# Kernel optimization log

Hardware: AMD Instinct MI355X
Metric: run time of the kernel (lower is better)

The kernel has to match this reference:

```python
import jax, jax.numpy as jnp
import numpy as np
from jax import lax

B = 128
NODES = 304
T_STEPS = 20
HID = 64
GCN_IN = 20
N = B * NODES            # 38912 graph nodes
E = N * 16               # 622592 edges
BN_EPS = 1e-5


def setup_inputs() -> dict:
    key = jax.random.key(0)
    ks = jax.random.split(key, 32)
    rn = lambda k, s, sc=0.1: jax.random.normal(k, s, jnp.float32) * sc
    return {
        "data_x": jax.random.normal(ks[0], (N, GCN_IN), jnp.float32),
        "edge_index": jax.random.randint(ks[1], (2, E), 0, N),
        "edge_weight": jax.random.uniform(ks[2], (E,), jnp.float32),
        "tc1_w1": rn(ks[3], (HID, 1, 1, 3)), "tc1_b1": rn(ks[4], (HID,)),
        "tc1_w2": rn(ks[5], (HID, 1, 1, 3)), "tc1_b2": rn(ks[6], (HID,)),
        "tc1_w3": rn(ks[7], (HID, 1, 1, 3)), "tc1_b3": rn(ks[8], (HID,)),
        "gcn_W0": rn(ks[9], (GCN_IN, HID)), "gcn_b0": rn(ks[10], (HID,)),
        "bn0_g": jax.random.uniform(ks[11], (HID,), jnp.float32, 0.5, 1.5), "bn0_b": rn(ks[12], (HID,)),
        "gcn_W1": rn(ks[13], (HID, HID)), "gcn_b1": rn(ks[14], (HID,)),
        "bn1_g": jax.random.uniform(ks[15], (HID,), jnp.float32, 0.5, 1.5), "bn1_b": rn(ks[16], (HID,)),
        "tc2_w1": rn(ks[17], (1, HID, 1, 3)), "tc2_b1": rn(ks[18], (1,)),
        "tc2_w2": rn(ks[19], (1, HID, 1, 3)), "tc2_b2": rn(ks[20], (1,)),
        "tc2_w3": rn(ks[21], (1, HID, 1, 3)), "tc2_b3": rn(ks[22], (1,)),
        "bn2d_g": jax.random.uniform(ks[23], (NODES,), jnp.float32, 0.5, 1.5), "bn2d_b": rn(ks[24], (NODES,)),
        "fc_W": rn(ks[25], (21 * NODES, 2048), 0.01), "fc_b": rn(ks[26], (2048,)),
        "fc4_W": rn(ks[27], (2048, 300), 0.01), "fc4_b": rn(ks[28], (300,)),
    }


def _bn(x, g, b):
    # eval-mode BatchNorm with fresh running stats (mean=0, var=1)
    return x * (g / jnp.sqrt(1.0 + BN_EPS)) + b


def _temporal_conv(X, w1, b1, w2, b2, w3, b3):
    # X: [B, T, nodes, C] -> permute to NCHW [B, C, nodes, T]
    Xp = jnp.transpose(X, (0, 3, 2, 1))
    conv = lambda w, b: lax.conv_general_dilated(
        Xp, w, (1, 1), [(0, 0), (1, 1)],
        dimension_numbers=("NCHW", "OIHW", "NCHW")) + b[None, :, None, None]
    P = conv(w1, b1)
    Q = jax.nn.sigmoid(conv(w2, b2))
    H = jax.nn.relu(P * Q + conv(w3, b3))
    return jnp.transpose(H, (0, 3, 2, 1))  # back to [B, T, nodes, C_out]


def reference(data_x, edge_index, edge_weight,
              tc1_w1, tc1_b1, tc1_w2, tc1_b2, tc1_w3, tc1_b3,
              gcn_W0, gcn_b0, bn0_g, bn0_b,
              gcn_W1, gcn_b1, bn1_g, bn1_b,
              tc2_w1, tc2_b1, tc2_w2, tc2_b2, tc2_w3, tc2_b3,
              bn2d_g, bn2d_b, fc_W, fc_b, fc4_W, fc4_b):
    n = data_x.shape[0]
    b = n // NODES

    # ---- GCN norm (sym, self-loops w=1) ----
    row, col = edge_index[0], edge_index[1]
    loop = jnp.arange(n)
    rowF = jnp.concatenate([row, loop])
    colF = jnp.concatenate([col, loop])
    ewF = jnp.concatenate([edge_weight, jnp.ones((n,), data_x.dtype)])
    deg = jax.ops.segment_sum(ewF, colF, num_segments=n)
    dinv = lax.rsqrt(jnp.maximum(deg, 1e-12))
    norm = dinv[rowF] * ewF * dinv[colF]

    def gconv(x, W, bias):
        h = x @ W
        return jax.ops.segment_sum(h[rowF] * norm[:, None], colF, num_segments=n) + bias

    x = jax.nn.relu(_bn(gconv(data_x, gcn_W0, gcn_b0), bn0_g, bn0_b))
    x = jax.nn.relu(_bn(gconv(x, gcn_W1, gcn_b1), bn1_g, bn1_b))  # [N, HID]

    # ---- temporal conv 1 ----
    X = data_x.reshape(b, T_STEPS, NODES, 1)
    T0 = _temporal_conv(X, tc1_w1, tc1_b1, tc1_w2, tc1_b2, tc1_w3, tc1_b3)  # [B,20,304,HID]

    # gcn_feature.permute(1,0).reshape(-1, 1, nodes, HID)
    gfeat = x.T.reshape(b, 1, NODES, HID)

    T = jnp.concatenate([jax.nn.relu(T0), gfeat], axis=1)  # [B, 21, 304, HID]
    T = jax.nn.relu(T)

    # ---- temporal conv 2 ----
    T = _temporal_conv(T, tc2_w1, tc2_b1, tc2_w2, tc2_b2, tc2_w3, tc2_b3)  # [B,21,304,1]

    # BatchNorm2d over node channel (axis=2 here), eval-mode running stats
    T = T * (bn2d_g / jnp.sqrt(1.0 + BN_EPS))[None, None, :, None] + bn2d_b[None, None, :, None]

    T = T.reshape(b, -1)  # [B, 6384]
    T = jax.nn.relu(T @ fc_W + fc_b)
    return T @ fc4_W + fc4_b  # [B, 300]
```

## Files before the change

kernel.cpp:

```cpp
#include <hip/hip_runtime.h>

#define NODES   304
#define BATCH   128
#define TSTEPS  20
#define HID     64
#define GCNIN   20
#define NN      (BATCH*NODES)
#define NE      (NN*16)
#define SEGSZ   (NN/4)
#define BCAP    64
#define FC1_IN  (21*NODES)
#define KP1     6400
#define FC1_OUT 2048
#define FC2_OUT 300
#define NP2     304
#define BN_EPS  1e-5f

typedef __attribute__((ext_vector_type(8))) short short8;
typedef __attribute__((ext_vector_type(4))) float f32x4;
typedef __attribute__((ext_vector_type(2))) float f32x2;

static __device__ __forceinline__ short f2bf(float x) {
    unsigned u = __float_as_uint(x);
    unsigned r = (u + 0x7FFF + ((u >> 16) & 1)) >> 16;
    return (short)r;
}
static __device__ __forceinline__ float bf2f(unsigned short v) {
    return __uint_as_float((unsigned)v << 16);
}

static __device__ __forceinline__ float fast_sigmoid(float q) {
    return __builtin_amdgcn_rcpf(1.f + __expf(-q));
}

static __device__ __forceinline__ f32x2 pk_fma(f32x2 a, f32x2 b, f32x2 c) {
    f32x2 d;
    asm("v_pk_fma_f32 %0, %1, %2, %3" : "=v"(d) : "v"(a), "v"(b), "v"(c));
    return d;
}

template <int C>
static __device__ __forceinline__ float dppadd(float v) {
    return v + __int_as_float(
        __builtin_amdgcn_update_dpp(0, __float_as_int(v), C, 0xF, 0xF, false));
}
static __device__ __forceinline__ float rsum16(float v) {
    v = dppadd<0x128>(v);
    v = dppadd<0x124>(v);
    v = dppadd<0x122>(v);
    v = dppadd<0x121>(v);
    return v;
}

__global__ void k_bucket(const int* __restrict__ ei, const float* __restrict__ ew,
                         int* __restrict__ cnt, int2* __restrict__ bucket) {
    int e = blockIdx.x * blockDim.x + threadIdx.x;
    if (e < NE) {
        int c = ei[NE + e];
        int slot = atomicAdd(&cnt[c], 1);
        if (slot < BCAP) {
            int2 v;
            v.x = ei[e];
            v.y = __float_as_int(ew[e]);
            bucket[((size_t)c << 6) + slot] = v;
        }
    }
}

__global__ __launch_bounds__(256) void k_mm20(const float* __restrict__ X,
                                              const float* __restrict__ W,
                                              const int* __restrict__ cnt,
                                              const int2* __restrict__ bucket,
                                              unsigned short* __restrict__ H,
                                              float* __restrict__ dinv) {
    int wv = threadIdx.x >> 6, f = threadIdx.x & 63;
    int n = blockIdx.x * 4 + wv;
    __shared__ float xs[4][GCNIN];
    __shared__ float rs[4][4];

    int2 be = bucket[((size_t)n << 6) + f];
    int deg = cnt[n];
    if (f < GCNIN) xs[wv][f] = X[(size_t)n * GCNIN + f];

    int dcap = deg < BCAP ? deg : BCAP;
    float wsum = (f < dcap) ? __int_as_float(be.y) : 0.f;
    wsum = rsum16(wsum);
    if ((f & 15) == 0) rs[wv][f >> 4] = wsum;
    __syncthreads();

    float dv = rsqrtf(fmaxf(1.f + rs[wv][0] + rs[wv][1] + rs[wv][2] + rs[wv][3],
                            1e-12f));
    if (f == 0) dinv[n] = dv;

    float acc = 0.f;
#pragma unroll
    for (int k = 0; k < GCNIN; k++) acc = fmaf(xs[wv][k], W[k * HID + f], acc);
    H[(size_t)n * HID + f] = (unsigned short)f2bf(acc * dv);
}

static __device__ __forceinline__ void stage_partition(
    int deg, int2 e, int f, int wv, int (*sIdx)[BCAP], float (*sWt)[BCAP],
    int& dcap) {
    dcap = deg < BCAP ? deg : BCAP;
    bool valid = f < dcap;
    int row = e.x;
    float w = __int_as_float(e.y);
    int q = (row >= SEGSZ) + (row >= 2 * SEGSZ) + (row >= 3 * SEGSZ);
    unsigned long long b0 = __ballot(valid && q == 0);
    unsigned long long b1 = __ballot(valid && q == 1);
    unsigned long long b2 = __ballot(valid && q == 2);
    unsigned long long b3 = __ballot(valid && q == 3);
    unsigned long long lmask = (1ULL << f) - 1;
    int pos = 0;
    if (q > 0) pos += __popcll(b0);
    if (q > 1) pos += __popcll(b1);
    if (q > 2) pos += __popcll(b2);
    unsigned long long mybal = (q == 0) ? b0 : (q == 1) ? b1 : (q == 2) ? b2 : b3;
    pos += __popcll(mybal & lmask);
    if (valid) {
        sIdx[wv][pos] = row;
        sWt[wv][pos] = w;
    }
}

__global__ __launch_bounds__(256) void k_gatherA(const int* __restrict__ cnt,
                                                 const int2* __restrict__ bucket,
                                                 const float* __restrict__ dinv,
                                                 const unsigned short* __restrict__ H0,
                                                 const float* __restrict__ gb,
                                                 const float* __restrict__ bng,
                                                 const float* __restrict__ bnb,
                                                 const float* __restrict__ W1,
                                                 unsigned short* __restrict__ H1) {
    int wv = threadIdx.x >> 6, f = threadIdx.x & 63;
    int c = blockIdx.x * 4 + wv;
    __shared__ int sIdx[4][BCAP];
    __shared__ float sWt[4][BCAP];
    __shared__ float xs[4][HID];

    int2 be = bucket[((size_t)c << 6) + f];
    int deg = cnt[c];
    float dc = dinv[c];
    float self = bf2f(H0[(size_t)c * HID + f]);

    int dcap;
    stage_partition(deg, be, f, wv, sIdx, sWt, dcap);
    __syncthreads();

    float acc = self;
    for (int base = 0; base < dcap; base += 16) {
        int idx[16];
        float w[16];
#pragma unroll
        for (int i = 0; i < 16; i++) {
            int l = (base + i < dcap) ? base + i : dcap - 1;
            idx[i] = sIdx[wv][l];
            w[i] = (base + i < dcap) ? sWt[wv][l] : 0.f;
        }
        float v[16];
#pragma unroll
        for (int i = 0; i < 16; i++) v[i] = bf2f(H0[(size_t)idx[i] * HID + f]);
#pragma unroll
        for (int i = 0; i < 16; i++) acc = fmaf(v[i], w[i], acc);
    }
    float scale = bng[f] * rsqrtf(1.f + BN_EPS);
    float y = fmaxf(fmaf(acc * dc + gb[f], scale, bnb[f]), 0.f);

    xs[wv][f] = y;
    __syncthreads();
    float h = 0.f;
#pragma unroll
    for (int k4 = 0; k4 < HID / 4; k4++) {
        float4 xv = *(const float4*)&xs[wv][k4 * 4];
        h = fmaf(xv.x, W1[(k4 * 4 + 0) * HID + f], h);
        h = fmaf(xv.y, W1[(k4 * 4 + 1) * HID + f], h);
        h = fmaf(xv.z, W1[(k4 * 4 + 2) * HID + f], h);
        h = fmaf(xv.w, W1[(k4 * 4 + 3) * HID + f], h);
    }
    H1[(size_t)c * HID + f] = (unsigned short)f2bf(h * dc);
}

__global__ __launch_bounds__(256) void k_gatherB(const int* __restrict__ cnt,
                                                 const int2* __restrict__ bucket,
                                                 const float* __restrict__ dinv,
                                                 const unsigned short* __restrict__ H,
                                                 const float* __restrict__ gb,
                                                 const float* __restrict__ bng,
                                                 const float* __restrict__ bnb,
                                                 float* __restrict__ XO) {
    int wv = threadIdx.x >> 6, f = threadIdx.x & 63;
    int c = blockIdx.x * 4 + wv;
    __shared__ int sIdx[4][BCAP];
    __shared__ float sWt[4][BCAP];

    int2 be = bucket[((size_t)c << 6) + f];
    int deg = cnt[c];
    float dc = dinv[c];
    float self = bf2f(H[(size_t)c * HID + f]);

    int dcap;
    stage_partition(deg, be, f, wv, sIdx, sWt, dcap);
    __syncthreads();

    float acc = self;
    for (int base = 0; base < dcap; base += 16) {
        int idx[16];
        float w[16];
#pragma unroll
        for (int i = 0; i < 16; i++) {
            int l = (base + i < dcap) ? base + i : dcap - 1;
            idx[i] = sIdx[wv][l];
            w[i] = (base + i < dcap) ? sWt[wv][l] : 0.f;
        }
        float v[16];
#pragma unroll
        for (int i = 0; i < 16; i++) v[i] = bf2f(H[(size_t)idx[i] * HID + f]);
#pragma unroll
        for (int i = 0; i < 16; i++) acc = fmaf(v[i], w[i], acc);
    }
    float scale = bng[f] * rsqrtf(1.f + BN_EPS);
    XO[(size_t)c * HID + f] = fmaxf(fmaf(acc * dc + gb[f], scale, bnb[f]), 0.f);
}

__global__ __launch_bounds__(256) void k_xpose(const float* __restrict__ x2,
                                               float* __restrict__ x2t) {
    __shared__ float tile[64][65];
    int n0 = blockIdx.x * 64;
    for (int i = threadIdx.x; i < 4096; i += 256) {
        int r = i >> 6, h = i & 63;
        tile[r][h] = x2[(size_t)(n0 + r) * 64 + h];
    }
    __syncthreads();
    for (int i = threadIdx.x; i < 4096; i += 256) {
        int h = i >> 6, c = i & 63;
        x2t[(size_t)h * NN + n0 + c] = tile[c][h];
    }
}

static __device__ __forceinline__ void load12(const float* base, f32x2 P[2][3]) {
    float4 f0 = *(const float4*)(base);
    float4 f1 = *(const float4*)(base + 4);
    float4 f2 = *(const float4*)(base + 8);
    P[0][0][0] = f0.x; P[0][0][1] = f0.w;
    P[0][1][0] = f0.y; P[0][1][1] = f1.x;
    P[0][2][0] = f0.z; P[0][2][1] = f1.y;
    P[1][0][0] = f1.z; P[1][0][1] = f2.y;
    P[1][1][0] = f1.w; P[1][1][1] = f2.z;
    P[1][2][0] = f2.x; P[1][2][1] = f2.w;
}

__global__ __launch_bounds__(256) void k_temporal2(
    const float* __restrict__ data_x, const float* __restrict__ x2t,
    const float* __restrict__ w1, const float* __restrict__ b1,
    const float* __restrict__ w2, const float* __restrict__ b2,
    const float* __restrict__ w3, const float* __restrict__ b3,
    const float* __restrict__ v1, const float* __restrict__ vb1,
    const float* __restrict__ v2, const float* __restrict__ vb2,
    const float* __restrict__ v3, const float* __restrict__ vb3,
    const float* __restrict__ bn2g, const float* __restrict__ bn2b,
    short* __restrict__ Ab) {
    int bn0 = blockIdx.x * 16;
    int b = bn0 / NODES, node0 = bn0 % NODES;
    int tid = threadIdx.x;
    int p = tid >> 4;
    int c0 = (tid & 15) << 2;
    int node = node0 + p;

    __shared__ float xs[16][22];
    __shared__ float wlds[1344];

    if (tid < 192) {
        wlds[tid] = w1[tid];
        wlds[192 + tid] = w2[tid];
        wlds[384 + tid] = w3[tid];
        wlds[576 + tid] = v1[tid];
        wlds[768 + tid] = v2[tid];
        wlds[960 + tid] = v3[tid];
    }
    if (tid < 64) {
        wlds[1152 + tid] = b1[tid];
        wlds[1216 + tid] = b2[tid];
        wlds[1280 + tid] = b3[tid];
    }
    for (int i = tid; i < 320; i += 256) {
        int t = i >> 4, pp = i & 15;
        xs[pp][t + 1] = data_x[b * (TSTEPS * NODES) + t * NODES + node0 + pp];
    }
    if (tid < 16) { xs[tid][0] = 0.f; xs[tid][21] = 0.f; }

    float cb1 = vb1[0], cb2 = vb2[0], cb3 = vb3[0];
    float s2 = bn2g[node] * rsqrtf(1.f + BN_EPS);
    float bb2 = bn2b[node];
    short* dst = Ab + (size_t)b * KP1;

    __syncthreads();

    f32x2 A1p[2][3], A2p[2][3], A3p[2][3], B1p[2], B2p[2], B3p[2];
    f32x2 U1p[2][3], U2p[2][3], U3p[2][3];
    load12(&wlds[0 + c0 * 3], A1p);
    load12(&wlds[192 + c0 * 3], A2p);
    load12(&wlds[384 + c0 * 3], A3p);
    load12(&wlds[576 + c0 * 3], U1p);
    load12(&wlds[768 + c0 * 3], U2p);
    load12(&wlds[960 + c0 * 3], U3p);
    {
        float4 t1 = *(const float4*)&wlds[1152 + c0];
        float4 t2 = *(const float4*)&wlds[1216 + c0];
        float4 t3 = *(const float4*)&wlds[1280 + c0];
        B1p[0][0] = t1.x; B1p[0][1] = t1.y; B1p[1][0] = t1.z; B1p[1][1] = t1.w;
        B2p[0][0] = t2.x; B2p[0][1] = t2.y; B2p[1][0] = t2.z; B2p[1][1] = t2.w;
        B3p[0][0] = t3.x; B3p[0][1] = t3.y; B3p[1][0] = t3.z; B3p[1][1] = t3.w;
    }

    f32x2 hA2[2] = {}, hB2[2] = {}, hC2[2];
    float xr0 = xs[p][0], xr1 = xs[p][1];

#pragma unroll
    for (int j = 0; j <= 21; j++) {
        if (j < 20) {
            float xr2 = xs[p][j + 2];
            f32x2 x0d, x1d, x2d;
            x0d[0] = xr0; x0d[1] = xr0;
            x1d[0] = xr1; x1d[1] = xr1;
            x2d[0] = xr2; x2d[1] = xr2;
#pragma unroll
            for (int cp = 0; cp < 2; cp++) {
                f32x2 pv = pk_fma(A1p[cp][2], x2d,
                            pk_fma(A1p[cp][1], x1d, pk_fma(A1p[cp][0], x0d, B1p[cp])));
                f32x2 qv = pk_fma(A2p[cp][2], x2d,
                            pk_fma(A2p[cp][1], x1d, pk_fma(A2p[cp][0], x0d, B2p[cp])));
                f32x2 rv = pk_fma(A3p[cp][2], x2d,
                            pk_fma(A3p[cp][1], x1d, pk_fma(A3p[cp][0], x0d, B3p[cp])));
                hC2[cp][0] = fmaxf(fmaf(pv[0], fast_sigmoid(qv[0]), rv[0]), 0.f);
                hC2[cp][1] = fmaxf(fmaf(pv[1], fast_sigmoid(qv[1]), rv[1]), 0.f);
            }
            xr0 = xr1;
            xr1 = xr2;
        } else if (j == 20) {
            const float4 gv = *(const float4*)(x2t + (size_t)(b >> 1) * NN +
                                               (b & 1) * (NODES * HID) + node * HID + c0);
            hC2[0][0] = fmaxf(gv.x, 0.f);
            hC2[0][1] = fmaxf(gv.y, 0.f);
            hC2[1][0] = fmaxf(gv.z, 0.f);
            hC2[1][1] = fmaxf(gv.w, 0.f);
        } else {
            hC2[0][0] = 0.f; hC2[0][1] = 0.f;
            hC2[1][0] = 0.f; hC2[1][1] = 0.f;
        }
        if (j >= 1) {
            int w = j - 1;
            f32x2 pa, qa, ra;
            pa[0] = 0.f; pa[1] = 0.f;
            qa[0] = 0.f; qa[1] = 0.f;
            ra[0] = 0.f; ra[1] = 0.f;
#pragma unroll
            for (int cp = 0; cp < 2; cp++) {
                pa = pk_fma(U1p[cp][0], hA2[cp], pa);
                pa = pk_fma(U1p[cp][1], hB2[cp], pa);
                pa = pk_fma(U1p[cp][2], hC2[cp], pa);
                qa = pk_fma(U2p[cp][0], hA2[cp], qa);
                qa = pk_fma(U2p[cp][1], hB2[cp], qa);
                qa = pk_fma(U2p[cp][2], hC2[cp], qa);
                ra = pk_fma(U3p[cp][0], hA2[cp], ra);
                ra = pk_fma(U3p[cp][1], hB2[cp], ra);
                ra = pk_fma(U3p[cp][2], hC2[cp], ra);
            }
            float pp_ = rsum16(pa[0] + pa[1]);
            float qq_ = rsum16(qa[0] + qa[1]);
            float rr_ = rsum16(ra[0] + ra[1]);
            float P = pp_ + cb1, Q = qq_ + cb2, R = rr_ + cb3;
            float hv = fmaxf(fmaf(P, fast_sigmoid(Q), R), 0.f);
            if ((tid & 15) == 0) dst[w * NODES + node] = f2bf(fmaf(hv, s2, bb2));
        }
        hA2[0] = hB2[0]; hA2[1] = hB2[1];
        hB2[0] = hC2[0]; hB2[1] = hC2[1];
    }
}

__global__ __launch_bounds__(256) void k_cvtW4(const float* __restrict__ W,
                                               short* __restrict__ Wt) {
    __shared__ float t[32][33];
    int tx = threadIdx.x & 31, ty = threadIdx.x >> 5;
    int n0 = blockIdx.x * 32, k0 = blockIdx.y * 32;
#pragma unroll
    for (int r = 0; r < 32; r += 8) {
        int k = k0 + r + ty, n = n0 + tx;
        t[r + ty][tx] = (n < FC2_OUT) ? W[(size_t)k * FC2_OUT + n] : 0.f;
    }
    __syncthreads();
#pragma unroll
    for (int r = 0; r < 32; r += 8) {
        int n = n0 + r + ty;
        if (n < NP2) Wt[(size_t)n * FC1_OUT + k0 + tx] = f2bf(t[tx][r + ty]);
    }
}

#define KSPL1 8
#define KCH1  (KP1 / KSPL1)
__global__ __launch_bounds__(256) void k_gemm1f(const short* __restrict__ Ab,
                                                const float* __restrict__ fcW,
                                                float* __restrict__ part) {
    int lane = threadIdx.x & 63, wv = threadIdx.x >> 6;
    int r = lane & 15, kg = lane >> 4;
    int nb = blockIdx.x * 64, sp = blockIdx.y;

    f32x4 acc[2][4] = {};
    const short* a0 = Ab + (size_t)(wv * 32 + r) * KP1;
    const short* a1 = a0 + (size_t)16 * KP1;

    int k0 = sp * KCH1 + kg * 8;
    const float* wp = fcW + (size_t)k0 * FC1_OUT + nb + r;
    bool tailblk = (sp == KSPL1 - 1);

#pragma unroll 1
    for (int s = 0; s < KCH1 / 32; s++, k0 += 32) {
        short8 av0 = *(const short8*)(a0 + k0);
        short8 av1 = *(const short8*)(a1 + k0);
        short8 bv[4];
        if (tailblk && s == KCH1 / 32 - 1) {
#pragma unroll
            for (int f = 0; f < 4; f++)
#pragma unroll
                for (int i = 0; i < 8; i++) {
                    float v = (k0 + i < FC1_IN) ? wp[(size_t)i * FC1_OUT + f * 16] : 0.f;
                    bv[f][i] = f2bf(v);
                }
        } else {
#pragma unroll
            for (int f = 0; f < 4; f++)
#pragma unroll
                for (int i = 0; i < 8; i++)
                    bv[f][i] = f2bf(wp[(size_t)i * FC1_OUT + f * 16]);
        }
        acc[0][0] = __builtin_amdgcn_mfma_f32_16x16x32_bf16(av0, bv[0], acc[0][0], 0, 0, 0);
        acc[1][0] = __builtin_amdgcn_mfma_f32_16x16x32_bf16(av1, bv[0], acc[1][0], 0, 0, 0);
        acc[0][1] = __builtin_amdgcn_mfma_f32_16x16x32_bf16(av0, bv[1], acc[0][1], 0, 0, 0);
        acc[1][1] = __builtin_amdgcn_mfma_f32_16x16x32_bf16(av1, bv[1], acc[1][1], 0, 0, 0);
        acc[0][2] = __builtin_amdgcn_mfma_f32_16x16x32_bf16(av0, bv[2], acc[0][2], 0, 0, 0);
        acc[1][2] = __builtin_amdgcn_mfma_f32_16x16x32_bf16(av1, bv[2], acc[1][2], 0, 0, 0);
        acc[0][3] = __builtin_amdgcn_mfma_f32_16x16x32_bf16(av0, bv[3], acc[0][3], 0, 0, 0);
        acc[1][3] = __builtin_amdgcn_mfma_f32_16x16x32_bf16(av1, bv[3], acc[1][3], 0, 0, 0);
        wp += (size_t)32 * FC1_OUT;
    }

    float* dst = part + (size_t)sp * BATCH * FC1_OUT;
#pragma unroll
    for (int m = 0; m < 2; m++)
#pragma unroll
        for (int f = 0; f < 4; f++)
#pragma unroll
            for (int j = 0; j < 4; j++) {
                int row = wv * 32 + m * 16 + kg * 4 + j;
                int col = nb + f * 16 + r;
                dst[(size_t)row * FC1_OUT + col] = acc[m][f][j];
            }
}

__global__ __launch_bounds__(256) void k_reduce1(const float* __restrict__ part,
                                                 const float* __restrict__ bias,
                                                 short* __restrict__ Ab2) {
    int idx = blockIdx.x * 256 + threadIdx.x;
    int o = idx & (FC1_OUT - 1);
    float s = bias[o];
#pragma unroll
    for (int sp = 0; sp < KSPL1; sp++) s += part[(size_t)sp * BATCH * FC1_OUT + idx];
    Ab2[idx] = f2bf(fmaxf(s, 0.f));
}

#define KSPL2 8
#define KCH2  (FC1_OUT / KSPL2)
__global__ __launch_bounds__(256) void k_gemm2(const short* __restrict__ Ab,
                                               const short* __restrict__ Wt,
                                               float* __restrict__ part) {
    int lane = threadIdx.x & 63, wv = threadIdx.x >> 6;
    int r = lane & 15, kg = lane >> 4;
    int nb = blockIdx.x * 16, sp = blockIdx.y;

    f32x4 acc[2] = {};
    const short* a0 = Ab + (size_t)(wv * 32 + r) * FC1_OUT;
    const short* a1 = a0 + (size_t)16 * FC1_OUT;
    const short* bp = Wt + (size_t)(nb + r) * FC1_OUT;

    int k0 = sp * KCH2 + kg * 8;
#pragma unroll
    for (int s = 0; s < KCH2 / 32; s++, k0 += 32) {
        short8 av0 = *(const short8*)(a0 + k0);
        short8 av1 = *(const short8*)(a1 + k0);
        short8 bv = *(const short8*)(bp + k0);
        acc[0] = __builtin_amdgcn_mfma_f32_16x16x32_bf16(av0, bv, acc[0], 0, 0, 0);
        acc[1] = __builtin_amdgcn_mfma_f32_16x16x32_bf16(av1, bv, acc[1], 0, 0, 0);
    }

    float* dst = part + (size_t)sp * BATCH * NP2;
#pragma unroll
    for (int m = 0; m < 2; m++)
#pragma unroll
        for (int j = 0; j < 4; j++) {
            int row = wv * 32 + m * 16 + kg * 4 + j;
            int col = nb + r;
            dst[(size_t)row * NP2 + col] = acc[m][j];
        }
}

__global__ __launch_bounds__(256) void k_reduce2(const float* __restrict__ part,
                                                 const float* __restrict__ bias,
                                                 float* __restrict__ out) {
    int idx = blockIdx.x * 256 + threadIdx.x;
    if (idx >= BATCH * NP2) return;
    int b = idx / NP2, o = idx % NP2;
    float s = 0.f;
#pragma unroll
    for (int sp = 0; sp < KSPL2; sp++) s += part[(size_t)sp * BATCH * NP2 + idx];
    if (o < FC2_OUT) out[(size_t)b * FC2_OUT + o] = s + bias[o];
}

extern "C" void kernel_launch(void* const* d_in, const int* in_sizes, int n_in,
                              void* d_out, int out_size, void* d_ws, size_t ws_size,
                              hipStream_t stream) {
    const float* data_x = (const float*)d_in[0];
    const int* ei = (const int*)d_in[1];
    const float* ew = (const float*)d_in[2];
    const float* tc1w1 = (const float*)d_in[3];
    const float* tc1b1 = (const float*)d_in[4];
    const float* tc1w2 = (const float*)d_in[5];
    const float* tc1b2 = (const float*)d_in[6];
    const float* tc1w3 = (const float*)d_in[7];
    const float* tc1b3 = (const float*)d_in[8];
    const float* W0 = (const float*)d_in[9];
    const float* gb0 = (const float*)d_in[10];
    const float* bn0g = (const float*)d_in[11];
    const float* bn0b = (const float*)d_in[12];
    const float* W1 = (const float*)d_in[13];
    const float* gb1 = (const float*)d_in[14];
    const float* bn1g = (const float*)d_in[15];
    const float* bn1b = (const float*)d_in[16];
    const float* tc2w1 = (const float*)d_in[17];
    const float* tc2b1 = (const float*)d_in[18];
    const float* tc2w2 = (const float*)d_in[19];
    const float* tc2b2 = (const float*)d_in[20];
    const float* tc2w3 = (const float*)d_in[21];
    const float* tc2b3 = (const float*)d_in[22];
    const float* bn2g = (const float*)d_in[23];
    const float* bn2b = (const float*)d_in[24];
    const float* fcW = (const float*)d_in[25];
    const float* fcb = (const float*)d_in[26];
    const float* fc4W = (const float*)d_in[27];
    const float* fc4b = (const float*)d_in[28];
    float* out = (float*)d_out;

    char* ws = (char*)d_ws;
    float* x2 = (float*)(ws + 0);
    short* Ab = (short*)(ws + 9961472);
    const size_t ARENA = 9961472 + 1638400;

    size_t off = ARENA;
    auto alloc = [&](size_t bytes) -> void* {
        void* p = ws + off;
        off = (off + bytes + 255) & ~(size_t)255;
        return p;
    };
    int2* bucket = (int2*)alloc((size_t)NN * BCAP * 8);
    int* cnt = (int*)alloc((size_t)NN * 4);
    float* dinv = (float*)alloc((size_t)NN * 4);
    unsigned short* h0 = (unsigned short*)alloc((size_t)NN * HID * 2);
    unsigned short* h1 = (unsigned short*)alloc((size_t)NN * HID * 2);

    float* x2t = (float*)(ws + ARENA);

    off = ARENA;
    float* part1 = (float*)alloc((size_t)KSPL1 * BATCH * FC1_OUT * 4);
    short* Ab2 = (short*)alloc((size_t)BATCH * FC1_OUT * 2);
    short* W4t = (short*)alloc((size_t)NP2 * FC1_OUT * 2);
    float* part2 = (float*)alloc((size_t)KSPL2 * BATCH * NP2 * 4);
    (void)ws_size; (void)in_sizes; (void)n_in; (void)out_size;

    hipMemsetAsync(cnt, 0, (size_t)NN * 4, stream);
    k_bucket<<<(NE + 255) / 256, 256, 0, stream>>>(ei, ew, cnt, bucket);

    k_mm20<<<NN / 4, 256, 0, stream>>>(data_x, W0, cnt, bucket, h0, dinv);
    k_gatherA<<<NN / 4, 256, 0, stream>>>(cnt, bucket, dinv, h0, gb0, bn0g, bn0b,
                                          W1, h1);
    k_gatherB<<<NN / 4, 256, 0, stream>>>(cnt, bucket, dinv, h1, gb1, bn1g, bn1b, x2);

    k_xpose<<<NN / 64, 256, 0, stream>>>(x2, x2t);

    hipMemsetAsync(Ab, 0, (size_t)BATCH * KP1 * 2, stream);
    k_temporal2<<<NN / 16, 256, 0, stream>>>(data_x, x2t, tc1w1, tc1b1, tc1w2, tc1b2,
                                             tc1w3, tc1b3, tc2w1, tc2b1, tc2w2, tc2b2,
                                             tc2w3, tc2b3, bn2g, bn2b, Ab);

    {
        dim3 g(FC1_OUT / 64, KSPL1);
        k_gemm1f<<<g, 256, 0, stream>>>(Ab, fcW, part1);
    }
    k_reduce1<<<BATCH * FC1_OUT / 256, 256, 0, stream>>>(part1, fcb, Ab2);
    {
        dim3 g((NP2 + 31) / 32, FC1_OUT / 32);
        k_cvtW4<<<g, 256, 0, stream>>>(fc4W, W4t);
    }
    {
        dim3 g(NP2 / 16, KSPL2);
        k_gemm2<<<g, 256, 0, stream>>>(Ab2, W4t, part2);
    }
    k_reduce2<<<(BATCH * NP2 + 255) / 256, 256, 0, stream>>>(part2, fc4b, out);
}
```

Before: 205.7 us.

## Aggregate raw 20-dim features before W0 and vectorize neighbor gathers

```diff
diff --git a/kernel.cpp b/kernel.cpp
--- a/kernel.cpp
+++ b/kernel.cpp
@@ -67,35 +67,31 @@
     }
 }
 
-__global__ __launch_bounds__(256) void k_mm20(const float* __restrict__ X,
-                                              const float* __restrict__ W,
+__global__ __launch_bounds__(256) void k_cvtX(const float* __restrict__ X,
                                               const int* __restrict__ cnt,
                                               const int2* __restrict__ bucket,
-                                              unsigned short* __restrict__ H,
+                                              unsigned short* __restrict__ Xb,
                                               float* __restrict__ dinv) {
-    int wv = threadIdx.x >> 6, f = threadIdx.x & 63;
-    int n = blockIdx.x * 4 + wv;
-    __shared__ float xs[4][GCNIN];
-    __shared__ float rs[4][4];
-
-    int2 be = bucket[((size_t)n << 6) + f];
+    int wv = threadIdx.x >> 5, f = threadIdx.x & 31;
+    int n = blockIdx.x * 8 + wv;
+    __shared__ float rs[8][2];
+
+    int2 e0 = bucket[((size_t)n << 6) + f];
+    int2 e1 = bucket[((size_t)n << 6) + 32 + f];
     int deg = cnt[n];
-    if (f < GCNIN) xs[wv][f] = X[(size_t)n * GCNIN + f];
+    float xv = (f < GCNIN) ? X[(size_t)n * GCNIN + f] : 0.f;
 
     int dcap = deg < BCAP ? deg : BCAP;
-    float wsum = (f < dcap) ? __int_as_float(be.y) : 0.f;
-    wsum = rsum16(wsum);
-    if ((f & 15) == 0) rs[wv][f >> 4] = wsum;
-    __syncthreads();
-
-    float dv = rsqrtf(fmaxf(1.f + rs[wv][0] + rs[wv][1] + rs[wv][2] + rs[wv][3],
-                            1e-12f));
+    float s = ((f < dcap) ? __int_as_float(e0.y) : 0.f) +
+              ((32 + f < dcap) ? __int_as_float(e1.y) : 0.f);
+    s = rsum16(s);
+    if ((f & 15) == 0) rs[wv][f >> 4] = s;
+    __syncthreads();
+
+    float dv = rsqrtf(fmaxf(1.f + rs[wv][0] + rs[wv][1], 1e-12f));
     if (f == 0) dinv[n] = dv;
-
-    float acc = 0.f;
-#pragma unroll
-    for (int k = 0; k < GCNIN; k++) acc = fmaf(xs[wv][k], W[k * HID + f], acc);
-    H[(size_t)n * HID + f] = (unsigned short)f2bf(acc * dv);
+    Xb[(size_t)n * 32 + f] = (f < GCNIN) ? (unsigned short)f2bf(xv * dv)
+                                         : (unsigned short)0;
 }
 
 static __device__ __forceinline__ void stage_partition(
@@ -123,48 +119,71 @@
     }
 }
 
-__global__ __launch_bounds__(256) void k_gatherA(const int* __restrict__ cnt,
-                                                 const int2* __restrict__ bucket,
-                                                 const float* __restrict__ dinv,
-                                                 const unsigned short* __restrict__ H0,
-                                                 const float* __restrict__ gb,
-                                                 const float* __restrict__ bng,
-                                                 const float* __restrict__ bnb,
-                                                 const float* __restrict__ W1,
-                                                 unsigned short* __restrict__ H1) {
+__global__ __launch_bounds__(256) void k_gather20(const int* __restrict__ cnt,
+                                                  const int2* __restrict__ bucket,
+                                                  const float* __restrict__ dinv,
+                                                  const unsigned short* __restrict__ Xb,
+                                                  const float* __restrict__ W0,
+                                                  const float* __restrict__ gb,
+                                                  const float* __restrict__ bng,
+                                                  const float* __restrict__ bnb,
+                                                  const float* __restrict__ W1,
+                                                  unsigned short* __restrict__ H1) {
     int wv = threadIdx.x >> 6, f = threadIdx.x & 63;
     int c = blockIdx.x * 4 + wv;
+    int g = f >> 4, r = f & 15;
     __shared__ int sIdx[4][BCAP];
     __shared__ float sWt[4][BCAP];
+    __shared__ float agg[4][32];
     __shared__ float xs[4][HID];
 
     int2 be = bucket[((size_t)c << 6) + f];
     int deg = cnt[c];
     float dc = dinv[c];
-    float self = bf2f(H0[(size_t)c * HID + f]);
+    unsigned selfv = *(const unsigned*)(Xb + (size_t)c * 32 + 2 * r);
 
     int dcap;
     stage_partition(deg, be, f, wv, sIdx, sWt, dcap);
     __syncthreads();
 
-    float acc = self;
+    f32x2 acc2;
+    acc2[0] = 0.f;
+    acc2[1] = 0.f;
     for (int base = 0; base < dcap; base += 16) {
-        int idx[16];
-        float w[16];
-#pragma unroll
-        for (int i = 0; i < 16; i++) {
-            int l = (base + i < dcap) ? base + i : dcap - 1;
-            idx[i] = sIdx[wv][l];
-            w[i] = (base + i < dcap) ? sWt[wv][l] : 0.f;
-        }
-        float v[16];
-#pragma unroll
-        for (int i = 0; i < 16; i++) v[i] = bf2f(H0[(size_t)idx[i] * HID + f]);
-#pragma unroll
-        for (int i = 0; i < 16; i++) acc = fmaf(v[i], w[i], acc);
-    }
+        int idx[4];
+        float w[4];
+#pragma unroll
+        for (int i = 0; i < 4; i++) {
+            int l = base + (i << 2) + g;
+            int lc = (l < dcap) ? l : dcap - 1;
+            idx[i] = sIdx[wv][lc];
+            w[i] = (l < dcap) ? sWt[wv][lc] : 0.f;
+        }
+        unsigned vv[4];
+#pragma unroll
+        for (int i = 0; i < 4; i++)
+            vv[i] = *(const unsigned*)(Xb + (size_t)idx[i] * 32 + 2 * r);
+#pragma unroll
+        for (int i = 0; i < 4; i++) {
+            acc2[0] = fmaf(bf2f((unsigned short)(vv[i] & 0xffff)), w[i], acc2[0]);
+            acc2[1] = fmaf(bf2f((unsigned short)(vv[i] >> 16)), w[i], acc2[1]);
+        }
+    }
+    acc2[0] += __shfl_xor(acc2[0], 16);
+    acc2[0] += __shfl_xor(acc2[0], 32);
+    acc2[1] += __shfl_xor(acc2[1], 16);
+    acc2[1] += __shfl_xor(acc2[1], 32);
+    if (g == 0) {
+        agg[wv][2 * r] = acc2[0] + bf2f((unsigned short)(selfv & 0xffff));
+        agg[wv][2 * r + 1] = acc2[1] + bf2f((unsigned short)(selfv >> 16));
+    }
+    __syncthreads();
+
+    float v = 0.f;
+#pragma unroll
+    for (int k = 0; k < GCNIN; k++) v = fmaf(agg[wv][k], W0[k * HID + f], v);
     float scale = bng[f] * rsqrtf(1.f + BN_EPS);
-    float y = fmaxf(fmaf(acc * dc + gb[f], scale, bnb[f]), 0.f);
+    float y = fmaxf(fmaf(v * dc + gb[f], scale, bnb[f]), 0.f);
 
     xs[wv][f] = y;
     __syncthreads();
@@ -190,36 +209,59 @@
                                                  float* __restrict__ XO) {
     int wv = threadIdx.x >> 6, f = threadIdx.x & 63;
     int c = blockIdx.x * 4 + wv;
+    int g = f >> 4, r = f & 15;
     __shared__ int sIdx[4][BCAP];
     __shared__ float sWt[4][BCAP];
 
     int2 be = bucket[((size_t)c << 6) + f];
     int deg = cnt[c];
     float dc = dinv[c];
-    float self = bf2f(H[(size_t)c * HID + f]);
+    ushort4 selfv = *(const ushort4*)(H + (size_t)c * HID + 4 * r);
 
     int dcap;
     stage_partition(deg, be, f, wv, sIdx, sWt, dcap);
     __syncthreads();
 
-    float acc = self;
+    float a0 = 0.f, a1 = 0.f, a2 = 0.f, a3 = 0.f;
     for (int base = 0; base < dcap; base += 16) {
-        int idx[16];
-        float w[16];
-#pragma unroll
-        for (int i = 0; i < 16; i++) {
-            int l = (base + i < dcap) ? base + i : dcap - 1;
-            idx[i] = sIdx[wv][l];
-            w[i] = (base + i < dcap) ? sWt[wv][l] : 0.f;
-        }
-        float v[16];
-#pragma unroll
-        for (int i = 0; i < 16; i++) v[i] = bf2f(H[(size_t)idx[i] * HID + f]);
-#pragma unroll
-        for (int i = 0; i < 16; i++) acc = fmaf(v[i], w[i], acc);
-    }
-    float scale = bng[f] * rsqrtf(1.f + BN_EPS);
-    XO[(size_t)c * HID + f] = fmaxf(fmaf(acc * dc + gb[f], scale, bnb[f]), 0.f);
+        int idx[4];
+        float w[4];
+#pragma unroll
+        for (int i = 0; i < 4; i++) {
+            int l = base + (i << 2) + g;
+            int lc = (l < dcap) ? l : dcap - 1;
+            idx[i] = sIdx[wv][lc];
+            w[i] = (l < dcap) ? sWt[wv][lc] : 0.f;
+        }
+        ushort4 hv[4];
+#pragma unroll
+        for (int i = 0; i < 4; i++)
+            hv[i] = *(const ushort4*)(H + (size_t)idx[i] * HID + 4 * r);
+#pragma unroll
+        for (int i = 0; i < 4; i++) {
+            a0 = fmaf(bf2f(hv[i].x), w[i], a0);
+            a1 = fmaf(bf2f(hv[i].y), w[i], a1);
+            a2 = fmaf(bf2f(hv[i].z), w[i], a2);
+            a3 = fmaf(bf2f(hv[i].w), w[i], a3);
+        }
+    }
+    a0 += __shfl_xor(a0, 16); a0 += __shfl_xor(a0, 32);
+    a1 += __shfl_xor(a1, 16); a1 += __shfl_xor(a1, 32);
+    a2 += __shfl_xor(a2, 16); a2 += __shfl_xor(a2, 32);
+    a3 += __shfl_xor(a3, 16); a3 += __shfl_xor(a3, 32);
+
+    if (g == 0) {
+        float4 scv = *(const float4*)&bng[4 * r];
+        float4 bbv = *(const float4*)&bnb[4 * r];
+        float4 gbv = *(const float4*)&gb[4 * r];
+        float rr = rsqrtf(1.f + BN_EPS);
+        float4 o;
+        o.x = fmaxf(fmaf((a0 + bf2f(selfv.x)) * dc + gbv.x, scv.x * rr, bbv.x), 0.f);
+        o.y = fmaxf(fmaf((a1 + bf2f(selfv.y)) * dc + gbv.y, scv.y * rr, bbv.y), 0.f);
+        o.z = fmaxf(fmaf((a2 + bf2f(selfv.z)) * dc + gbv.z, scv.z * rr, bbv.z), 0.f);
+        o.w = fmaxf(fmaf((a3 + bf2f(selfv.w)) * dc + gbv.w, scv.w * rr, bbv.w), 0.f);
+        *(float4*)(XO + (size_t)c * HID + 4 * r) = o;
+    }
 }
 
 __global__ __launch_bounds__(256) void k_xpose(const float* __restrict__ x2,
@@ -562,7 +604,7 @@
     int2* bucket = (int2*)alloc((size_t)NN * BCAP * 8);
     int* cnt = (int*)alloc((size_t)NN * 4);
     float* dinv = (float*)alloc((size_t)NN * 4);
-    unsigned short* h0 = (unsigned short*)alloc((size_t)NN * HID * 2);
+    unsigned short* Xb = (unsigned short*)alloc((size_t)NN * 32 * 2);
     unsigned short* h1 = (unsigned short*)alloc((size_t)NN * HID * 2);
 
     float* x2t = (float*)(ws + ARENA);
@@ -577,9 +619,9 @@
     hipMemsetAsync(cnt, 0, (size_t)NN * 4, stream);
     k_bucket<<<(NE + 255) / 256, 256, 0, stream>>>(ei, ew, cnt, bucket);
 
-    k_mm20<<<NN / 4, 256, 0, stream>>>(data_x, W0, cnt, bucket, h0, dinv);
-    k_gatherA<<<NN / 4, 256, 0, stream>>>(cnt, bucket, dinv, h0, gb0, bn0g, bn0b,
-                                          W1, h1);
+    k_cvtX<<<NN / 8, 256, 0, stream>>>(data_x, cnt, bucket, Xb, dinv);
+    k_gather20<<<NN / 4, 256, 0, stream>>>(cnt, bucket, dinv, Xb, W0, gb0, bn0g,
+                                           bn0b, W1, h1);
     k_gatherB<<<NN / 4, 256, 0, stream>>>(cnt, bucket, dinv, h1, gb1, bn1g, bn1b, x2);
 
     k_xpose<<<NN / 64, 256, 0, stream>>>(x2, x2t);
```

Result: faster. 190.7 us (-7.3%).
